# Kernel tuning notes

Measured on AMD Instinct MI355X. Metric: run time of the kernel, lower is better.

The kernel has to match this reference:

```python
import jax, jax.numpy as jnp
import numpy as np

N = 12500      # nodes
E = 200000     # edges (avg degree 16)
IN = 32        # inp_dim
OUT = 32       # out_dim
ATTN = 32      # attn_rel_emb_dim
R = 200        # num_rels
NB = 50        # num_bases


def setup_inputs() -> dict:
    key = jax.random.key(0)
    ks = jax.random.split(key, 10)
    node_feat = jax.random.normal(ks[0], (N, IN), jnp.float32)
    total_edge = jax.random.randint(ks[1], (2, E), 0, N)
    total_target_relation = jax.random.normal(ks[2], (E, ATTN), jnp.float32)
    total_relation_embed = jax.random.normal(ks[3], (E, ATTN), jnp.float32)
    total_relation = jax.random.randint(ks[4], (E,), 0, R)
    # learned parameters (xavier-ish scale)
    weight = jax.random.normal(ks[5], (NB, IN, OUT), jnp.float32) * 0.1
    w_comp = jax.random.normal(ks[6], (R, NB), jnp.float32) * 0.1
    self_loop_weight = jax.random.normal(ks[7], (IN, OUT), jnp.float32) * 0.1
    A_w = jax.random.normal(ks[8], (IN, 2 * IN + 2 * ATTN), jnp.float32) * 0.1
    A_b = jnp.zeros((IN,), jnp.float32)
    B_w = jax.random.normal(ks[9], (1, IN), jnp.float32) * 0.1
    B_b = jnp.zeros((1,), jnp.float32)
    return {
        'node_feat': node_feat,
        'total_target_relation': total_target_relation,
        'total_relation_embed': total_relation_embed,
        'weight': weight,
        'w_comp': w_comp,
        'self_loop_weight': self_loop_weight,
        'A_w': A_w,
        'A_b': A_b,
        'B_w': B_w,
        'B_b': B_b,
        'total_edge': total_edge,
        'total_relation': total_relation,
    }


def reference(node_feat, total_target_relation, total_relation_embed,
              weight, w_comp, self_loop_weight, A_w, A_b, B_w, B_b,
              total_edge, total_relation):
    # basis decomposition: per-relation weight [R, IN, OUT]
    rel_w = jnp.einsum('rb,bio->rio', w_comp, weight)
    src = node_feat[total_edge[0]]            # [E, IN]
    tgt = node_feat[total_edge[1]]            # [E, IN]
    # per-edge relation-specific transform (bmm in torch)
    msg = jnp.einsum('ei,eio->eo', src, rel_w[total_relation])  # [E, OUT]
    curr = tgt @ self_loop_weight             # [E, OUT]
    # attention MLP: sigmoid(B(relu(A(concat))))
    e = jnp.concatenate([src, tgt, total_relation_embed, total_target_relation], axis=1)
    h = jax.nn.relu(e @ A_w.T + A_b)
    a = jax.nn.sigmoid(h @ B_w.T + B_b)       # [E, 1]
    curr = curr + msg * a
    # gnn_spmm(e2n_sp, curr): scatter-add edge messages to target nodes
    out = jax.ops.segment_sum(curr, total_edge[1], num_segments=node_feat.shape[0])
    return out  # [N, OUT]
```

## Files before the change

### kernel.cpp

```cpp
#include <hip/hip_runtime.h>

#define N_NODES 12500
#define N_EDGES 200000
#define DIM 32
#define N_REL 200
#define N_BASES 50

#define OUT_ELEMS   (N_NODES * DIM)
#define ZERO_BLOCKS ((OUT_ELEMS + 1023) / 1024)

#define PE_MAX 203008
#define INIT_BLOCKS ((PE_MAX + 1023) / 1024)

#define NB_BLK 100
#define CHUNK ((N_EDGES + NB_BLK - 1) / NB_BLK)

#define AWBF_OFF  (N_REL * 1024 * 2)
#define SLWT_OFF  (AWBF_OFF + 32 * 128 * 2)
#define BC_OFF    (SLWT_OFF + 32 * 32 * 2)
#define BB_OFF    (BC_OFF + NB_BLK * N_REL * 4)
#define SLOT_OFF  (BB_OFF + NB_BLK * N_REL * 4)

typedef __attribute__((ext_vector_type(8))) short short8;
typedef __attribute__((ext_vector_type(4))) float f32x4;

__device__ __forceinline__ unsigned short f2bf(float x) {
    union { float f; unsigned u; } v; v.f = x;
    unsigned r = (v.u + 0x7FFFu + ((v.u >> 16) & 1u)) >> 16;
    return (unsigned short)r;
}

__device__ __forceinline__ short8 cvt8(float4 a, float4 b) {
    short8 r;
    r[0] = (short)f2bf(a.x); r[1] = (short)f2bf(a.y);
    r[2] = (short)f2bf(a.z); r[3] = (short)f2bf(a.w);
    r[4] = (short)f2bf(b.x); r[5] = (short)f2bf(b.y);
    r[6] = (short)f2bf(b.z); r[7] = (short)f2bf(b.w);
    return r;
}

#define MFMA(A, B, C) __builtin_amdgcn_mfma_f32_16x16x32_bf16(A, B, C, 0, 0, 0)

__global__ __launch_bounds__(256) void prep_kernel(
    const float* __restrict__ weight,
    const float* __restrict__ w_comp,
    const float* __restrict__ Aw,
    const float* __restrict__ slw,
    const int*  __restrict__ rel,
    unsigned short* __restrict__ relwT_bf,
    unsigned short* __restrict__ aw_bf,
    unsigned short* __restrict__ slwT_bf,
    int* __restrict__ blockCounts,
    int4* __restrict__ slot4,
    float* __restrict__ out)
{
    int b = blockIdx.x, tid = threadIdx.x;
    if (b < N_REL) {
        __shared__ float wc[N_BASES];
        if (tid < N_BASES) wc[tid] = w_comp[b * N_BASES + tid];
        __syncthreads();
        const float* wp = weight + tid * 4;
        float4 acc = make_float4(0.f, 0.f, 0.f, 0.f);
        #pragma unroll 10
        for (int bb = 0; bb < N_BASES; bb++) {
            float4 w = *(const float4*)(wp + bb * 1024);
            float c = wc[bb];
            acc.x = fmaf(c, w.x, acc.x); acc.y = fmaf(c, w.y, acc.y);
            acc.z = fmaf(c, w.z, acc.z); acc.w = fmaf(c, w.w, acc.w);
        }
        int i  = tid >> 3;
        int o0 = (tid * 4) & 31;
        unsigned short* dst = relwT_bf + b * 1024 + i;
        dst[(o0 + 0) * 32] = f2bf(acc.x);
        dst[(o0 + 1) * 32] = f2bf(acc.y);
        dst[(o0 + 2) * 32] = f2bf(acc.z);
        dst[(o0 + 3) * 32] = f2bf(acc.w);
    } else if (b < N_REL + ZERO_BLOCKS) {
        int base = (b - N_REL) * 1024 + tid * 4;
        if (base + 3 < OUT_ELEMS)
            *(float4*)(out + base) = make_float4(0.f, 0.f, 0.f, 0.f);
        else
            for (int k = 0; k < 4; k++)
                if (base + k < OUT_ELEMS) out[base + k] = 0.f;
    } else if (b == N_REL + ZERO_BLOCKS) {
        for (int x = tid; x < 32 * 128; x += 256) aw_bf[x] = f2bf(Aw[x]);
        for (int x = tid; x < 32 * 32; x += 256) {
            int i = x >> 5, j = x & 31;
            slwT_bf[j * 32 + i] = f2bf(slw[x]);
        }
    } else if (b < N_REL + ZERO_BLOCKS + 1 + INIT_BLOCKS) {
        int base = (b - (N_REL + ZERO_BLOCKS + 1)) * 1024 + tid * 4;
        #pragma unroll
        for (int k = 0; k < 4; k++) {
            int j = base + k;
            if (j < PE_MAX) slot4[j] = make_int4(0, -1, 0, 0);
        }
    } else {
        __shared__ int h[N_REL];
        int blk = b - (N_REL + ZERO_BLOCKS + 1 + INIT_BLOCKS);
        for (int x = tid; x < N_REL; x += 256) h[x] = 0;
        __syncthreads();
        int e0 = blk * CHUNK;
        int e1 = e0 + CHUNK; if (e1 > N_EDGES) e1 = N_EDGES;
        for (int e = e0 + tid; e < e1; e += 256) {
            int r = rel[e]; r = r < 0 ? 0 : (r >= N_REL ? N_REL - 1 : r);
            atomicAdd(&h[r], 1);
        }
        __syncthreads();
        for (int x = tid; x < N_REL; x += 256)
            blockCounts[blk * N_REL + x] = h[x];
    }
}

__global__ __launch_bounds__(256) void scan_kernel(
    const int* __restrict__ blockCounts, int* __restrict__ blockBase)
{
    __shared__ int tot[N_REL];
    __shared__ int off[N_REL];
    int tid = threadIdx.x;
    if (tid < N_REL) {
        int run = 0;
        for (int b = 0; b < NB_BLK; b++) run += blockCounts[b * N_REL + tid];
        tot[tid] = run;
    }
    __syncthreads();
    if (tid == 0) {
        int run = 0;
        for (int r = 0; r < N_REL; r++) {
            off[r] = run;
            run += (tot[r] + 15) & ~15;
        }
    }
    __syncthreads();
    if (tid < N_REL) {
        int run = off[tid];
        for (int b = 0; b < NB_BLK; b++) {
            blockBase[b * N_REL + tid] = run;
            run += blockCounts[b * N_REL + tid];
        }
    }
}

__global__ __launch_bounds__(256) void scatter_kernel(
    const int* __restrict__ edge0, const int* __restrict__ edge1,
    const int* __restrict__ rel,
    const int* __restrict__ blockBase,
    int4* __restrict__ slot4)
{
    __shared__ int cur[N_REL];
    int blk = blockIdx.x, tid = threadIdx.x;
    for (int x = tid; x < N_REL; x += 256) cur[x] = blockBase[blk * N_REL + x];
    __syncthreads();
    int e0 = blk * CHUNK;
    int e1 = e0 + CHUNK; if (e1 > N_EDGES) e1 = N_EDGES;
    for (int e = e0 + tid; e < e1; e += 256) {
        int r = rel[e];   r = r < 0 ? 0 : (r >= N_REL   ? N_REL   - 1 : r);
        int s = edge0[e]; s = s < 0 ? 0 : (s >= N_NODES ? N_NODES - 1 : s);
        int t = edge1[e]; t = t < 0 ? 0 : (t >= N_NODES ? N_NODES - 1 : t);
        int pos = atomicAdd(&cur[r], 1);
        slot4[pos] = make_int4(s, t, e, r);
    }
}

__global__ __launch_bounds__(256) void edge_kernel(
    const float* __restrict__ node_feat,
    const float* __restrict__ ttr,
    const float* __restrict__ tre,
    const float* __restrict__ Ab,
    const float* __restrict__ Bw,
    const float* __restrict__ Bb,
    const int4* __restrict__ slot4,
    const unsigned short* __restrict__ relwT_bf,
    const unsigned short* __restrict__ aw_bf,
    const unsigned short* __restrict__ slwT_bf,
    float* __restrict__ out)
{
    int tid  = threadIdx.x;
    int wave = tid >> 6;
    int lane = tid & 63;
    int m = lane & 15;
    int q = lane >> 4;
    int base = blockIdx.x * 64 + wave * 16;

    int s_ld = 0, t_ld = -1, e_ld = 0, r_ld = 0;
    if (lane < 16) {
        int4 v = slot4[base + lane];
        s_ld = v.x; t_ld = v.y; e_ld = v.z; r_ld = v.w;
    }
    int r_w = __shfl(r_ld, 0, 64);

    int s_m = __shfl(s_ld, m, 64);
    int t_m = __shfl(t_ld, m, 64);
    int e_m = __shfl(e_ld, m, 64);
    int t_mc = t_m < 0 ? 0 : t_m;

    const float* sp = node_feat + s_m * DIM + q * 8;
    float4 sv0 = *(const float4*)sp, sv1 = *(const float4*)(sp + 4);
    const float* tp = node_feat + t_mc * DIM + q * 8;
    float4 tv0 = *(const float4*)tp, tv1 = *(const float4*)(tp + 4);
    const float* rp = tre + e_m * DIM + q * 8;
    float4 rv0 = *(const float4*)rp, rv1 = *(const float4*)(rp + 4);
    const float* qp = ttr + e_m * DIM + q * 8;
    float4 qv0 = *(const float4*)qp, qv1 = *(const float4*)(qp + 4);

    short8 fsrc = cvt8(sv0, sv1);
    short8 ftgt = cvt8(tv0, tv1);
    short8 fre  = cvt8(rv0, rv1);
    short8 ftr  = cvt8(qv0, qv1);

    short8 bA[4][2], bS[2], bM[2];
    #pragma unroll
    for (int hh = 0; hh < 2; hh++) {
        #pragma unroll
        for (int c = 0; c < 4; c++)
            bA[c][hh] = *(const short8*)(aw_bf + (16 * hh + m) * 128 + 32 * c + 8 * q);
        bS[hh] = *(const short8*)(slwT_bf + (16 * hh + m) * 32 + 8 * q);
        bM[hh] = *(const short8*)(relwT_bf + r_w * 1024 + (16 * hh + m) * 32 + 8 * q);
    }

    float ab0 = Ab[m], ab1 = Ab[16 + m];
    f32x4 hacc0 = {ab0, ab0, ab0, ab0};
    f32x4 hacc1 = {ab1, ab1, ab1, ab1};
    f32x4 cacc0 = {0.f, 0.f, 0.f, 0.f};
    f32x4 cacc1 = {0.f, 0.f, 0.f, 0.f};
    f32x4 macc0 = {0.f, 0.f, 0.f, 0.f};
    f32x4 macc1 = {0.f, 0.f, 0.f, 0.f};

    hacc0 = MFMA(fsrc, bA[0][0], hacc0);  hacc1 = MFMA(fsrc, bA[0][1], hacc1);
    hacc0 = MFMA(ftgt, bA[1][0], hacc0);  hacc1 = MFMA(ftgt, bA[1][1], hacc1);
    hacc0 = MFMA(fre,  bA[2][0], hacc0);  hacc1 = MFMA(fre,  bA[2][1], hacc1);
    hacc0 = MFMA(ftr,  bA[3][0], hacc0);  hacc1 = MFMA(ftr,  bA[3][1], hacc1);
    cacc0 = MFMA(ftgt, bS[0], cacc0);     cacc1 = MFMA(ftgt, bS[1], cacc1);
    macc0 = MFMA(fsrc, bM[0], macc0);     macc1 = MFMA(fsrc, bM[1], macc1);

    float bw0 = Bw[m], bw1 = Bw[16 + m], Bb0 = Bb[0];
    float av[4];
    #pragma unroll
    for (int v = 0; v < 4; v++) {
        float p = fmaxf(hacc0[v], 0.f) * bw0 + fmaxf(hacc1[v], 0.f) * bw1;
        p += __shfl_xor(p, 1, 16);
        p += __shfl_xor(p, 2, 16);
        p += __shfl_xor(p, 4, 16);
        p += __shfl_xor(p, 8, 16);
        av[v] = 1.f / (1.f + __expf(-(p + Bb0)));
    }
    #pragma unroll
    for (int v = 0; v < 4; v++) {
        int row = 4 * q + v;
        int tv = __shfl(t_ld, row, 64);
        if (tv >= 0) {
            atomicAdd(&out[tv * DIM + m],      cacc0[v] + macc0[v] * av[v]);
            atomicAdd(&out[tv * DIM + 16 + m], cacc1[v] + macc1[v] * av[v]);
        }
    }
}

extern "C" void kernel_launch(void* const* d_in, const int* in_sizes, int n_in,
                              void* d_out, int out_size, void* d_ws, size_t ws_size,
                              hipStream_t stream) {
    const float* node_feat = (const float*)d_in[0];
    const float* ttr       = (const float*)d_in[1];
    const float* tre       = (const float*)d_in[2];
    const float* weight    = (const float*)d_in[3];
    const float* w_comp    = (const float*)d_in[4];
    const float* slw       = (const float*)d_in[5];
    const float* Aw        = (const float*)d_in[6];
    const float* Ab        = (const float*)d_in[7];
    const float* Bw        = (const float*)d_in[8];
    const float* Bb        = (const float*)d_in[9];
    const int*  total_edge = (const int*)d_in[10];
    const int*  rel        = (const int*)d_in[11];
    const int*  edge0 = total_edge;
    const int*  edge1 = total_edge + N_EDGES;

    char* ws = (char*)d_ws;
    unsigned short* relwT_bf = (unsigned short*)ws;
    unsigned short* aw_bf    = (unsigned short*)(ws + AWBF_OFF);
    unsigned short* slwT_bf  = (unsigned short*)(ws + SLWT_OFF);
    int*  blockCounts = (int*)(ws + BC_OFF);
    int*  blockBase   = (int*)(ws + BB_OFF);
    int4* slot4       = (int4*)(ws + SLOT_OFF);
    float* out = (float*)d_out;

    prep_kernel<<<N_REL + ZERO_BLOCKS + 1 + INIT_BLOCKS + NB_BLK, 256, 0, stream>>>(
        weight, w_comp, Aw, slw, rel, relwT_bf, aw_bf, slwT_bf,
        blockCounts, slot4, out);

    scan_kernel<<<1, 256, 0, stream>>>(blockCounts, blockBase);

    scatter_kernel<<<NB_BLK, 256, 0, stream>>>(
        edge0, edge1, rel, blockBase, slot4);

    edge_kernel<<<PE_MAX / 64, 256, 0, stream>>>(
        node_feat, ttr, tre, Ab, Bw, Bb,
        slot4, relwT_bf, aw_bf, slwT_bf, out);
}
```

Before: 157.0 us.

## Parallelize relation-sort scan, transpose block counts, write only padding slots

The counting sort of edges by relation now splits edges over 200 blocks of 1000 and stores per-block counts transposed, so the scan kernel reads them contiguously with int4 loads. The serial thread-0 prefix sum over relation totals becomes a shared-memory Hillis-Steele scan. Instead of pre-filling the whole slot array with dummy entries in the prep kernel, extra scatter blocks write dummies only into per-relation padding and the tail. This removes a full 3 MB initialization pass and shortens the single-block scan, at the cost of hardcoding the chunk size to divide the edge count exactly.

```diff
diff --git a/kernel.cpp b/kernel.cpp
--- a/kernel.cpp
+++ b/kernel.cpp
@@ -10,16 +10,18 @@
 #define ZERO_BLOCKS ((OUT_ELEMS + 1023) / 1024)
 
 #define PE_MAX 203008
-#define INIT_BLOCKS ((PE_MAX + 1023) / 1024)
-
-#define NB_BLK 100
-#define CHUNK ((N_EDGES + NB_BLK - 1) / NB_BLK)
+#define N_DUMMY_BLOCKS 8
+
+#define NB_BLK 200
+#define CHUNK 1000
 
 #define AWBF_OFF  (N_REL * 1024 * 2)
 #define SLWT_OFF  (AWBF_OFF + 32 * 128 * 2)
-#define BC_OFF    (SLWT_OFF + 32 * 32 * 2)
-#define BB_OFF    (BC_OFF + NB_BLK * N_REL * 4)
-#define SLOT_OFF  (BB_OFF + NB_BLK * N_REL * 4)
+#define BCT_OFF   (SLWT_OFF + 32 * 32 * 2)
+#define BBT_OFF   (BCT_OFF + N_REL * NB_BLK * 4)
+#define OFFS_OFF  (BBT_OFF + N_REL * NB_BLK * 4)
+#define TOTS_OFF  (OFFS_OFF + 816)
+#define SLOT_OFF  (TOTS_OFF + 800)
 
 typedef __attribute__((ext_vector_type(8))) short short8;
 typedef __attribute__((ext_vector_type(4))) float f32x4;
@@ -50,8 +52,7 @@
     unsigned short* __restrict__ relwT_bf,
     unsigned short* __restrict__ aw_bf,
     unsigned short* __restrict__ slwT_bf,
-    int* __restrict__ blockCounts,
-    int4* __restrict__ slot4,
+    int* __restrict__ blockCountsT,
     float* __restrict__ out)
 {
     int b = blockIdx.x, tid = threadIdx.x;
@@ -88,55 +89,68 @@
             int i = x >> 5, j = x & 31;
             slwT_bf[j * 32 + i] = f2bf(slw[x]);
         }
-    } else if (b < N_REL + ZERO_BLOCKS + 1 + INIT_BLOCKS) {
-        int base = (b - (N_REL + ZERO_BLOCKS + 1)) * 1024 + tid * 4;
-        #pragma unroll
-        for (int k = 0; k < 4; k++) {
-            int j = base + k;
-            if (j < PE_MAX) slot4[j] = make_int4(0, -1, 0, 0);
-        }
     } else {
         __shared__ int h[N_REL];
-        int blk = b - (N_REL + ZERO_BLOCKS + 1 + INIT_BLOCKS);
+        int blk = b - (N_REL + ZERO_BLOCKS + 1);
         for (int x = tid; x < N_REL; x += 256) h[x] = 0;
         __syncthreads();
         int e0 = blk * CHUNK;
-        int e1 = e0 + CHUNK; if (e1 > N_EDGES) e1 = N_EDGES;
-        for (int e = e0 + tid; e < e1; e += 256) {
+        for (int e = e0 + tid; e < e0 + CHUNK; e += 256) {
             int r = rel[e]; r = r < 0 ? 0 : (r >= N_REL ? N_REL - 1 : r);
             atomicAdd(&h[r], 1);
         }
         __syncthreads();
         for (int x = tid; x < N_REL; x += 256)
-            blockCounts[blk * N_REL + x] = h[x];
+            blockCountsT[x * NB_BLK + blk] = h[x];
     }
 }
 
 __global__ __launch_bounds__(256) void scan_kernel(
-    const int* __restrict__ blockCounts, int* __restrict__ blockBase)
+    const int* __restrict__ blockCountsT,
+    int* __restrict__ blockBaseT,
+    int* __restrict__ offs, int* __restrict__ tots)
 {
-    __shared__ int tot[N_REL];
-    __shared__ int off[N_REL];
+    __shared__ int s0[256];
+    __shared__ int pval[256];
     int tid = threadIdx.x;
+    int tot = 0;
     if (tid < N_REL) {
-        int run = 0;
-        for (int b = 0; b < NB_BLK; b++) run += blockCounts[b * N_REL + tid];
-        tot[tid] = run;
-    }
+        const int4* cp = (const int4*)(blockCountsT + tid * NB_BLK);
+        #pragma unroll 5
+        for (int b = 0; b < NB_BLK / 4; b++) {
+            int4 c = cp[b];
+            tot += c.x + c.y + c.z + c.w;
+        }
+    }
+    int p = (tid < N_REL) ? ((tot + 15) & ~15) : 0;
+    pval[tid] = p;
+    s0[tid] = p;
     __syncthreads();
-    if (tid == 0) {
-        int run = 0;
-        for (int r = 0; r < N_REL; r++) {
-            off[r] = run;
-            run += (tot[r] + 15) & ~15;
-        }
-    }
-    __syncthreads();
+    #pragma unroll
+    for (int d = 1; d < 256; d <<= 1) {
+        int v = s0[tid];
+        if (tid >= d) v += s0[tid - d];
+        __syncthreads();
+        s0[tid] = v;
+        __syncthreads();
+    }
+    int off = s0[tid] - pval[tid];
+    if (tid < N_REL) { offs[tid] = off; tots[tid] = tot; }
+    if (tid == 255) offs[N_REL] = s0[255];
     if (tid < N_REL) {
-        int run = off[tid];
-        for (int b = 0; b < NB_BLK; b++) {
-            blockBase[b * N_REL + tid] = run;
-            run += blockCounts[b * N_REL + tid];
+        const int4* cp = (const int4*)(blockCountsT + tid * NB_BLK);
+        int4* bp = (int4*)(blockBaseT + tid * NB_BLK);
+        int run = off;
+        #pragma unroll 5
+        for (int b = 0; b < NB_BLK / 4; b++) {
+            int4 c = cp[b];
+            int4 w;
+            w.x = run;
+            w.y = w.x + c.x;
+            w.z = w.y + c.y;
+            w.w = w.z + c.z;
+            run = w.w + c.w;
+            bp[b] = w;
         }
     }
 }
@@ -144,21 +158,37 @@
 __global__ __launch_bounds__(256) void scatter_kernel(
     const int* __restrict__ edge0, const int* __restrict__ edge1,
     const int* __restrict__ rel,
-    const int* __restrict__ blockBase,
+    const int* __restrict__ blockBaseT,
+    const int* __restrict__ offs, const int* __restrict__ tots,
     int4* __restrict__ slot4)
 {
-    __shared__ int cur[N_REL];
     int blk = blockIdx.x, tid = threadIdx.x;
-    for (int x = tid; x < N_REL; x += 256) cur[x] = blockBase[blk * N_REL + x];
-    __syncthreads();
-    int e0 = blk * CHUNK;
-    int e1 = e0 + CHUNK; if (e1 > N_EDGES) e1 = N_EDGES;
-    for (int e = e0 + tid; e < e1; e += 256) {
-        int r = rel[e];   r = r < 0 ? 0 : (r >= N_REL   ? N_REL   - 1 : r);
-        int s = edge0[e]; s = s < 0 ? 0 : (s >= N_NODES ? N_NODES - 1 : s);
-        int t = edge1[e]; t = t < 0 ? 0 : (t >= N_NODES ? N_NODES - 1 : t);
-        int pos = atomicAdd(&cur[r], 1);
-        slot4[pos] = make_int4(s, t, e, r);
+    if (blk < NB_BLK) {
+        __shared__ int cur[N_REL];
+        for (int x = tid; x < N_REL; x += 256)
+            cur[x] = blockBaseT[x * NB_BLK + blk];
+        __syncthreads();
+        int e0 = blk * CHUNK;
+        #pragma unroll
+        for (int e = e0 + tid; e < e0 + CHUNK; e += 256) {
+            int r = rel[e];   r = r < 0 ? 0 : (r >= N_REL   ? N_REL   - 1 : r);
+            int s = edge0[e]; s = s < 0 ? 0 : (s >= N_NODES ? N_NODES - 1 : s);
+            int t = edge1[e]; t = t < 0 ? 0 : (t >= N_NODES ? N_NODES - 1 : t);
+            int pos = atomicAdd(&cur[r], 1);
+            slot4[pos] = make_int4(s, t, e, r);
+        }
+    } else {
+        int db = blk - NB_BLK;
+        const int4 dummy = make_int4(0, -1, 0, 0);
+        for (int r = db; r < N_REL; r += N_DUMMY_BLOCKS) {
+            int start = offs[r] + tots[r];
+            int end   = offs[r] + ((tots[r] + 15) & ~15);
+            for (int j = start + tid; j < end; j += 256)
+                slot4[j] = dummy;
+        }
+        int padTotal = offs[N_REL];
+        for (int j = padTotal + db * 256 + tid; j < PE_MAX; j += N_DUMMY_BLOCKS * 256)
+            slot4[j] = dummy;
     }
 }
 
@@ -277,19 +307,21 @@
     unsigned short* relwT_bf = (unsigned short*)ws;
     unsigned short* aw_bf    = (unsigned short*)(ws + AWBF_OFF);
     unsigned short* slwT_bf  = (unsigned short*)(ws + SLWT_OFF);
-    int*  blockCounts = (int*)(ws + BC_OFF);
-    int*  blockBase   = (int*)(ws + BB_OFF);
-    int4* slot4       = (int4*)(ws + SLOT_OFF);
+    int*  blockCountsT = (int*)(ws + BCT_OFF);
+    int*  blockBaseT   = (int*)(ws + BBT_OFF);
+    int*  offs         = (int*)(ws + OFFS_OFF);
+    int*  tots         = (int*)(ws + TOTS_OFF);
+    int4* slot4        = (int4*)(ws + SLOT_OFF);
     float* out = (float*)d_out;
 
-    prep_kernel<<<N_REL + ZERO_BLOCKS + 1 + INIT_BLOCKS + NB_BLK, 256, 0, stream>>>(
+    prep_kernel<<<N_REL + ZERO_BLOCKS + 1 + NB_BLK, 256, 0, stream>>>(
         weight, w_comp, Aw, slw, rel, relwT_bf, aw_bf, slwT_bf,
-        blockCounts, slot4, out);
-
-    scan_kernel<<<1, 256, 0, stream>>>(blockCounts, blockBase);
-
-    scatter_kernel<<<NB_BLK, 256, 0, stream>>>(
-        edge0, edge1, rel, blockBase, slot4);
+        blockCountsT, out);
+
+    scan_kernel<<<1, 256, 0, stream>>>(blockCountsT, blockBaseT, offs, tots);
+
+    scatter_kernel<<<NB_BLK + N_DUMMY_BLOCKS, 256, 0, stream>>>(
+        edge0, edge1, rel, blockBaseT, offs, tots, slot4);
 
     edge_kernel<<<PE_MAX / 64, 256, 0, stream>>>(
         node_feat, ttr, tre, Ab, Bw, Bb,
```

Measured after the change: 160.0 us. About the same (+1.9%).
